# Kernel optimization log

Hardware: AMD Instinct MI355X
Metric: run time of the kernel (lower is better)

The kernel has to match this reference:

```python
import jax, jax.numpy as jnp
import numpy as np


def setup_inputs() -> dict:
    key = jax.random.key(0)
    k1, k2, k3 = jax.random.split(key, 3)
    B, S = 65536, 256
    sample_seq = jax.random.randint(k1, (B, S), 0, 20, dtype=jnp.int64 if jax.config.jax_enable_x64 else jnp.int32)
    sample_value = jax.random.normal(k2, (B, S), dtype=jnp.float32)
    sample_reward = jax.random.uniform(k3, (B, S), dtype=jnp.float32)
    return {"sample_seq": sample_seq, "sample_value": sample_value, "sample_reward": sample_reward}


def reference(sample_seq, sample_value, sample_reward):
    # 1) Zero out every token at-and-after the first 0 in each row
    #    (vectorized form of the original per-token Python loop).
    zero_seen = jnp.cumsum((sample_seq == 0).astype(jnp.int32), axis=1) > 0  # [B,S]
    masked_seq = jnp.where(zero_seen, 0, sample_seq)

    # 2) mask = (seq > 0) shifted right by one, with a leading column of ones.
    m = (masked_seq > 0).astype(jnp.float32)
    mask = jnp.concatenate([jnp.ones((m.shape[0], 1), dtype=m.dtype), m[:, :-1]], axis=1)

    # 3) Masked MSE between (detached) reward and predicted value.
    reward_diff = sample_reward - sample_value  # [B,S]
    output = reward_diff * reward_diff * mask
    loss = output.sum() / mask.sum()

    sample_mean = sample_reward.mean()  # stands in for the printed avg sample reward
    return (loss, reward_diff.mean(), sample_mean)
```

## Files before the change

### kernel.cpp

```cpp
#include <hip/hip_runtime.h>


__global__ __launch_bounds__(256, 2) void ac_mse_reduce(
    const int* __restrict__ seq,
    const float* __restrict__ value,
    const float* __restrict__ reward,
    double* __restrict__ part,
    int B, int nb) {

    const int S = 256;
    const int lane = threadIdx.x & 63;
    const int wv = threadIdx.x >> 6;
    const int wave = blockIdx.x * 4 + wv;
    const int T = nb * 4;

    double acc_sq = 0.0, acc_sd = 0.0, acc_sr = 0.0;
    int cnt = 0;
    const unsigned long long lmlt = (1ull << lane) - 1ull;

    const size_t step = (size_t)T * S;
    const size_t e0 = (size_t)wave * S + (size_t)(lane * 4);
    const int*   sp = seq + e0;
    const float* vp = value + e0;
    const float* rp = reward + e0;

    auto process = [&](const int4 s, const float4 v, const float4 r) {
        int p = 4;
        if (s.w == 0) p = 3;
        if (s.z == 0) p = 2;
        if (s.y == 0) p = 1;
        if (s.x == 0) p = 0;
        const unsigned long long zm = __ballot(p < 4);
        const int m = ((zm & lmlt) == 0) ? ((p < 4) ? p + 1 : 4) : 0;

        const float d0 = r.x - v.x;
        const float d1 = r.y - v.y;
        const float d2 = r.z - v.z;
        const float d3 = r.w - v.w;
        float lsq = 0.0f;
        if (m > 0) lsq += d0 * d0;
        if (m > 1) lsq += d1 * d1;
        if (m > 2) lsq += d2 * d2;
        if (m > 3) lsq += d3 * d3;

        cnt += m;
        acc_sq += (double)lsq;
        acc_sd += (double)((d0 + d1) + (d2 + d3));
        acc_sr += (double)((r.x + r.y) + (r.z + r.w));
    };

    const int niter = (wave < B) ? ((B - 1 - wave) / T + 1) : 0;
    int k = 0;
    for (; k + 4 <= niter; k += 4) {
        const int4   s0 = *reinterpret_cast<const int4*>(sp);
        const int4   s1 = *reinterpret_cast<const int4*>(sp + step);
        const int4   s2 = *reinterpret_cast<const int4*>(sp + 2 * step);
        const int4   s3 = *reinterpret_cast<const int4*>(sp + 3 * step);
        const float4 v0 = *reinterpret_cast<const float4*>(vp);
        const float4 v1 = *reinterpret_cast<const float4*>(vp + step);
        const float4 v2 = *reinterpret_cast<const float4*>(vp + 2 * step);
        const float4 v3 = *reinterpret_cast<const float4*>(vp + 3 * step);
        const float4 r0 = *reinterpret_cast<const float4*>(rp);
        const float4 r1 = *reinterpret_cast<const float4*>(rp + step);
        const float4 r2 = *reinterpret_cast<const float4*>(rp + 2 * step);
        const float4 r3 = *reinterpret_cast<const float4*>(rp + 3 * step);
        sp += 4 * step; vp += 4 * step; rp += 4 * step;
        process(s0, v0, r0);
        process(s1, v1, r1);
        process(s2, v2, r2);
        process(s3, v3, r3);
    }
    for (; k < niter; ++k) {
        const int4   s0 = *reinterpret_cast<const int4*>(sp);
        const float4 v0 = *reinterpret_cast<const float4*>(vp);
        const float4 r0 = *reinterpret_cast<const float4*>(rp);
        sp += step; vp += step; rp += step;
        process(s0, v0, r0);
    }

    double acc_cnt = (double)cnt;
    #pragma unroll
    for (int off = 32; off > 0; off >>= 1) {
        acc_sq  += __shfl_down(acc_sq,  off);
        acc_cnt += __shfl_down(acc_cnt, off);
        acc_sd  += __shfl_down(acc_sd,  off);
        acc_sr  += __shfl_down(acc_sr,  off);
    }

    __shared__ double sm[4][4];
    if (lane == 0) {
        sm[0][wv] = acc_sq;
        sm[1][wv] = acc_cnt;
        sm[2][wv] = acc_sd;
        sm[3][wv] = acc_sr;
    }
    __syncthreads();
    if (threadIdx.x == 0) {
        part[0 * (size_t)nb + blockIdx.x] = sm[0][0] + sm[0][1] + sm[0][2] + sm[0][3];
        part[1 * (size_t)nb + blockIdx.x] = sm[1][0] + sm[1][1] + sm[1][2] + sm[1][3];
        part[2 * (size_t)nb + blockIdx.x] = sm[2][0] + sm[2][1] + sm[2][2] + sm[2][3];
        part[3 * (size_t)nb + blockIdx.x] = sm[3][0] + sm[3][1] + sm[3][2] + sm[3][3];
    }
}

__global__ __launch_bounds__(256) void ac_mse_final(
    const double* __restrict__ part, float* __restrict__ out,
    int nb, double inv_n) {

    const int lane = threadIdx.x & 63;
    const int c = threadIdx.x >> 6;
    const double* p = part + (size_t)c * nb;

    double a0 = 0, a1 = 0, a2 = 0, a3 = 0;
    int b = lane;
    for (; b + 192 < nb; b += 256) {
        a0 += p[b]; a1 += p[b + 64]; a2 += p[b + 128]; a3 += p[b + 192];
    }
    for (; b < nb; b += 64) a0 += p[b];
    double a = (a0 + a1) + (a2 + a3);

    #pragma unroll
    for (int off = 32; off > 0; off >>= 1) a += __shfl_down(a, off);

    __shared__ double sm[4];
    if (lane == 0) sm[c] = a;
    __syncthreads();
    if (threadIdx.x == 0) {
        out[0] = (float)(sm[0] / sm[1]);
        out[1] = (float)(sm[2] * inv_n);
        out[2] = (float)(sm[3] * inv_n);
    }
}

extern "C" void kernel_launch(void* const* d_in, const int* in_sizes, int n_in,
                              void* d_out, int out_size, void* d_ws, size_t ws_size,
                              hipStream_t stream) {
    const int*   seq    = (const int*)d_in[0];
    const float* value  = (const float*)d_in[1];
    const float* reward = (const float*)d_in[2];
    float*  out = (float*)d_out;
    double* ws  = (double*)d_ws;

    const int S = 256;
    const long long total = (long long)in_sizes[0];
    const int B = (int)(total / S);

    int nb = 2048;
    while ((size_t)nb * 4 * sizeof(double) > ws_size && nb > 1) nb >>= 1;

    ac_mse_reduce<<<nb, 256, 0, stream>>>(seq, value, reward, ws, B, nb);
    ac_mse_final<<<1, 256, 0, stream>>>(ws, out, nb, 1.0 / (double)total);
}
```

Before: 39.99 us.

## Load only the first 64 seq tokens per row, scanning further on demand

Each row's first-zero position is now found from a ballot over only the first 64 sequence tokens, one int per lane. Further 64-token chunks are loaded only when no zero has appeared yet. With tokens drawn from 0-19, almost every row has a zero early, so most of the seq traffic (a third of all input bytes) is skipped. The cost is a data-dependent, possibly divergent extra loop, and the gain depends on the input distribution.

```diff
diff --git a/kernel.cpp b/kernel.cpp
--- a/kernel.cpp
+++ b/kernel.cpp
@@ -16,22 +16,27 @@
 
     double acc_sq = 0.0, acc_sd = 0.0, acc_sr = 0.0;
     int cnt = 0;
-    const unsigned long long lmlt = (1ull << lane) - 1ull;
 
     const size_t step = (size_t)T * S;
-    const size_t e0 = (size_t)wave * S + (size_t)(lane * 4);
-    const int*   sp = seq + e0;
-    const float* vp = value + e0;
-    const float* rp = reward + e0;
+    const int*   spl = seq + (size_t)wave * S + (size_t)lane;
+    const float* vp  = value + (size_t)wave * S + (size_t)(lane * 4);
+    const float* rp  = reward + (size_t)wave * S + (size_t)(lane * 4);
 
-    auto process = [&](const int4 s, const float4 v, const float4 r) {
-        int p = 4;
-        if (s.w == 0) p = 3;
-        if (s.z == 0) p = 2;
-        if (s.y == 0) p = 1;
-        if (s.x == 0) p = 0;
-        const unsigned long long zm = __ballot(p < 4);
-        const int m = ((zm & lmlt) == 0) ? ((p < 4) ? p + 1 : 4) : 0;
+    auto process = [&](int s0, const float4 v, const float4 r, const int* sq) {
+        unsigned long long bal = __ballot(s0 == 0);
+        int count;
+        if (bal) {
+            count = __ffsll(bal);
+        } else {
+            count = S;
+            for (int c = 1; c < S / 64; ++c) {
+                const int sc = sq[c * 64];
+                const unsigned long long b2 = __ballot(sc == 0);
+                if (b2) { count = c * 64 + (int)__ffsll(b2); break; }
+            }
+        }
+        int m = count - 4 * lane;
+        m = m < 0 ? 0 : (m > 4 ? 4 : m);
 
         const float d0 = r.x - v.x;
         const float d1 = r.y - v.y;
@@ -52,10 +57,10 @@
     const int niter = (wave < B) ? ((B - 1 - wave) / T + 1) : 0;
     int k = 0;
     for (; k + 4 <= niter; k += 4) {
-        const int4   s0 = *reinterpret_cast<const int4*>(sp);
-        const int4   s1 = *reinterpret_cast<const int4*>(sp + step);
-        const int4   s2 = *reinterpret_cast<const int4*>(sp + 2 * step);
-        const int4   s3 = *reinterpret_cast<const int4*>(sp + 3 * step);
+        const int    s0 = spl[0];
+        const int    s1 = spl[step];
+        const int    s2 = spl[2 * step];
+        const int    s3 = spl[3 * step];
         const float4 v0 = *reinterpret_cast<const float4*>(vp);
         const float4 v1 = *reinterpret_cast<const float4*>(vp + step);
         const float4 v2 = *reinterpret_cast<const float4*>(vp + 2 * step);
@@ -64,18 +69,18 @@
         const float4 r1 = *reinterpret_cast<const float4*>(rp + step);
         const float4 r2 = *reinterpret_cast<const float4*>(rp + 2 * step);
         const float4 r3 = *reinterpret_cast<const float4*>(rp + 3 * step);
-        sp += 4 * step; vp += 4 * step; rp += 4 * step;
-        process(s0, v0, r0);
-        process(s1, v1, r1);
-        process(s2, v2, r2);
-        process(s3, v3, r3);
+        process(s0, v0, r0, spl);
+        process(s1, v1, r1, spl + step);
+        process(s2, v2, r2, spl + 2 * step);
+        process(s3, v3, r3, spl + 3 * step);
+        spl += 4 * step; vp += 4 * step; rp += 4 * step;
     }
     for (; k < niter; ++k) {
-        const int4   s0 = *reinterpret_cast<const int4*>(sp);
+        const int    s0 = spl[0];
         const float4 v0 = *reinterpret_cast<const float4*>(vp);
         const float4 r0 = *reinterpret_cast<const float4*>(rp);
-        sp += step; vp += step; rp += step;
-        process(s0, v0, r0);
+        process(s0, v0, r0, spl);
+        spl += step; vp += step; rp += step;
     }
 
     double acc_cnt = (double)cnt;
```

New measurement: 33.18 us (median of 2 runs). -17.0%, faster.
